# Kernel tuning notes

Hardware: AMD Instinct MI355X
Metric: run time of the kernel (lower is better)

## Reference

```python
import jax, jax.numpy as jnp
import numpy as np

N = 100000   # nodes
E = 1000000  # directed edges
C = 64       # channels
K = 4        # propagation hops
DT = 1.0     # dt; exp_init=False branch: 2*x + dt^2*conv(x) - x_pre


def setup_inputs() -> dict:
    key = jax.random.key(0)
    k1, k2, k3, k4, k5 = jax.random.split(key, 5)
    x = jax.random.normal(k1, (N, C), dtype=jnp.float32)
    x_pre = jax.random.normal(k2, (N, C), dtype=jnp.float32)
    edge_index = jax.random.randint(k3, (2, E), 0, N, dtype=jnp.int32)
    bound = 1.0 / np.sqrt(C)  # PyG Linear default (kaiming-uniform-like)
    W = jax.random.uniform(k4, (C, C), jnp.float32, -bound, bound)
    b = jax.random.uniform(k5, (C,), jnp.float32, -bound, bound)
    return {"x": x, "x_pre": x_pre, "edge_index": edge_index, "W": W, "b": b}


def _sgc(x, edge_index, W, b):
    # gcn_norm: add self-loops, symmetric normalization D^-1/2 (A+I) D^-1/2
    loop = jnp.arange(N, dtype=edge_index.dtype)
    src = jnp.concatenate([edge_index[0], loop])  # source j
    dst = jnp.concatenate([edge_index[1], loop])  # target i
    deg = jax.ops.segment_sum(jnp.ones(src.shape, jnp.float32), dst, num_segments=N)
    dinv = jnp.where(deg > 0, jax.lax.rsqrt(deg), 0.0)
    norm = dinv[src] * dinv[dst]  # [E+N]
    h = x
    for _ in range(K):  # K-hop sparse propagation (gather -> scale -> scatter-add)
        h = jax.ops.segment_sum(h[src] * norm[:, None], dst, num_segments=N)
    return h @ W.T + b  # SGConv final linear


def reference(x, x_pre, edge_index, W, b):
    return 2.0 * x + (DT * DT) * _sgc(x, edge_index, W, b) - x_pre
```

## Files before the change

### kernel.cpp

```cpp
#include <hip/hip_runtime.h>
#include <hip/hip_fp16.h>

#define CCH 64
#define NBLK 128
#define BKT  256


__global__ void countA(const int* __restrict__ dst, int* __restrict__ cntmat,
                       int E, int chunk, int B) {
    __shared__ int h[512];
    int t = threadIdx.x, blk = blockIdx.x;
    for (int i = t; i < B; i += 256) h[i] = 0;
    __syncthreads();
    int e0 = blk * chunk, e1 = min(e0 + chunk, E);
    for (int e = e0 + t; e < e1; e += 256) atomicAdd(&h[dst[e] >> 8], 1);
    __syncthreads();
    for (int i = t; i < B; i += 256) cntmat[i * NBLK + blk] = h[i];
}

__global__ void scan1(const int* __restrict__ cnt, int* __restrict__ part,
                      int* __restrict__ bsum, int N) {
    __shared__ int s[256];
    int t = threadIdx.x;
    int base = blockIdx.x * 1024 + t * 4;
    int v0 = (base + 0 < N) ? cnt[base + 0] : 0;
    int v1 = (base + 1 < N) ? cnt[base + 1] : 0;
    int v2 = (base + 2 < N) ? cnt[base + 2] : 0;
    int v3 = (base + 3 < N) ? cnt[base + 3] : 0;
    s[t] = v0 + v1 + v2 + v3;
    __syncthreads();
    for (int off = 1; off < 256; off <<= 1) {
        int xx = (t >= off) ? s[t - off] : 0;
        __syncthreads();
        s[t] += xx;
        __syncthreads();
    }
    int excl = (t == 0) ? 0 : s[t - 1];
    if (t == 255) bsum[blockIdx.x] = s[255];
    if (base + 0 < N) part[base + 0] = excl;
    if (base + 1 < N) part[base + 1] = excl + v0;
    if (base + 2 < N) part[base + 2] = excl + v0 + v1;
    if (base + 3 < N) part[base + 3] = excl + v0 + v1 + v2;
}

__device__ __forceinline__ void scan_bsum(const int* __restrict__ bsum, int NB2,
                                          int* sbs, int t) {
    int v = (t < NB2) ? bsum[t] : 0;
    sbs[t] = v;
    __syncthreads();
    for (int o = 1; o < 256; o <<= 1) {
        int xx = (t >= o) ? sbs[t - o] : 0;
        __syncthreads();
        sbs[t] += xx;
        __syncthreads();
    }
    int e = sbs[t] - v;
    __syncthreads();
    sbs[t] = e;
    __syncthreads();
}

__global__ void partA(const int* __restrict__ src, const int* __restrict__ dst,
                      const int* __restrict__ part, const int* __restrict__ bsum,
                      unsigned* __restrict__ brec, int E, int chunk, int B, int NB2) {
    __shared__ int cur[512];
    __shared__ int sbs[256];
    int t = threadIdx.x, blk = blockIdx.x;
    scan_bsum(bsum, NB2, sbs, t);
    for (int i = t; i < B; i += 256) {
        int idx = i * NBLK + blk;
        cur[i] = part[idx] + sbs[idx >> 10];
    }
    __syncthreads();
    int e0 = blk * chunk, e1 = min(e0 + chunk, E);
    for (int e = e0 + t; e < e1; e += 256) {
        int s = src[e], d = dst[e];
        int pos = atomicAdd(&cur[d >> 8], 1);
        brec[pos] = ((unsigned)s << 8) | (unsigned)(d & 255);
    }
}

__global__ void buildB(const unsigned* __restrict__ brec, const int* __restrict__ part,
                       const int* __restrict__ bsum, int* __restrict__ row_ptr,
                       int* __restrict__ adj, float* __restrict__ dinv,
                       float* __restrict__ dinv2, const float* __restrict__ x,
                       __half* __restrict__ xh, int N, int B, int E, int NB2) {
    __shared__ int hist[256];
    __shared__ int scanbuf[256];
    __shared__ int cursor[256];
    __shared__ int sbs[256];
    __shared__ float sdinv[256];
    int t = threadIdx.x, k = blockIdx.x;
    scan_bsum(bsum, NB2, sbs, t);
    int i0 = k * NBLK;
    int base = part[i0] + sbs[i0 >> 10];
    int nextb;
    if (k + 1 < B) {
        int i1 = (k + 1) * NBLK;
        nextb = part[i1] + sbs[i1 >> 10];
    } else {
        nextb = E;
    }
    hist[t] = 0;
    __syncthreads();
    for (int i = base + t; i < nextb; i += 256) atomicAdd(&hist[brec[i] & 255u], 1);
    __syncthreads();
    int v = hist[t];
    scanbuf[t] = v;
    __syncthreads();
    for (int o = 1; o < 256; o <<= 1) {
        int xx = (t >= o) ? scanbuf[t - o] : 0;
        __syncthreads();
        scanbuf[t] += xx;
        __syncthreads();
    }
    int excl = scanbuf[t] - v;
    int node = k * 256 + t;
    float di = 0.f;
    if (node < N) {
        int p = base + excl;
        row_ptr[node] = p;
        cursor[t] = p;
        float dp1 = (float)v + 1.0f;
        di = rsqrtf(dp1);
        dinv[node]  = di;
        dinv2[node] = 1.0f / dp1;
    }
    sdinv[t] = di;
    if (k == 0 && t == 0) row_ptr[N] = E;
    __syncthreads();
    for (int i = base + t; i < nextb; i += 256) {
        unsigned r = brec[i];
        int pos = atomicAdd(&cursor[r & 255u], 1);
        adj[pos] = (int)(r >> 8);
    }
    int nodeBase = k * 256;
    for (int i = t; i < 2048; i += 256) {
        int nl = i >> 3;
        int node2 = nodeBase + nl;
        if (node2 < N) {
            float d = sdinv[nl];
            size_t baseE = (size_t)node2 * 64 + (size_t)(i & 7) * 8;
            float4 a = *(const float4*)&x[baseE];
            float4 c = *(const float4*)&x[baseE + 4];
            float4 o;
            __half2* op = (__half2*)&o;
            op[0] = __float22half2_rn(make_float2(d * a.x, d * a.y));
            op[1] = __float22half2_rn(make_float2(d * a.z, d * a.w));
            op[2] = __float22half2_rn(make_float2(d * c.x, d * c.y));
            op[3] = __float22half2_rn(make_float2(d * c.z, d * c.w));
            *(float4*)&xh[baseE] = o;
        }
    }
}


__device__ __forceinline__ void acc16w(float4 hv, float w, float* acc) {
    __half2* hp = (__half2*)&hv;
    #pragma unroll
    for (int i2 = 0; i2 < 4; ++i2) {
        float2 f = __half22float2(hp[i2]);
        acc[2 * i2]     = fmaf(w, f.x, acc[2 * i2]);
        acc[2 * i2 + 1] = fmaf(w, f.y, acc[2 * i2 + 1]);
    }
}

__device__ __forceinline__ void prop_body(const __half* __restrict__ hin,
                                          const int* __restrict__ row_ptr,
                                          const int* __restrict__ adj,
                                          int nodeC, int cnt, int g8, int q,
                                          int E, float* acc) {
    int rp0 = row_ptr[nodeC];

    int R = cnt;
    R = max(R, __shfl_xor(R, 8, 64));
    R = max(R, __shfl_xor(R, 16, 64));
    R = max(R, __shfl_xor(R, 32, 64));

    const float4* hin16 = (const float4*)hin;
    float4 selfv = hin16[(size_t)nodeC * 8 + q];

    int eCur = adj[rp0 + q];
    int eNxt = adj[rp0 + 8 + q];
    int j0 = __shfl(eCur, g8 + 0, 64); j0 = (0 < cnt) ? j0 : 0;
    int j1 = __shfl(eCur, g8 + 1, 64); j1 = (1 < cnt) ? j1 : 0;
    int j2 = __shfl(eCur, g8 + 2, 64); j2 = (2 < cnt) ? j2 : 0;
    int j3 = __shfl(eCur, g8 + 3, 64); j3 = (3 < cnt) ? j3 : 0;
    float4 gA0 = hin16[(size_t)j0 * 8 + q];
    float4 gA1 = hin16[(size_t)j1 * 8 + q];
    float4 gA2 = hin16[(size_t)j2 * 8 + q];
    float4 gA3 = hin16[(size_t)j3 * 8 + q];
    float4 gB0, gB1, gB2, gB3;

    acc16w(selfv, 1.f, acc);

    for (int r = 0; r < R; r += 8) {
        int t;
        t = r + 4; j0 = __shfl(eCur, g8 + (t & 7), 64); j0 = (t < cnt) ? j0 : 0;
        t = r + 5; j1 = __shfl(eCur, g8 + (t & 7), 64); j1 = (t < cnt) ? j1 : 0;
        t = r + 6; j2 = __shfl(eCur, g8 + (t & 7), 64); j2 = (t < cnt) ? j2 : 0;
        t = r + 7; j3 = __shfl(eCur, g8 + (t & 7), 64); j3 = (t < cnt) ? j3 : 0;
        gB0 = hin16[(size_t)j0 * 8 + q];
        gB1 = hin16[(size_t)j1 * 8 + q];
        gB2 = hin16[(size_t)j2 * 8 + q];
        gB3 = hin16[(size_t)j3 * 8 + q];
        float w;
        w = (r + 0 < cnt) ? 1.f : 0.f; acc16w(gA0, w, acc);
        w = (r + 1 < cnt) ? 1.f : 0.f; acc16w(gA1, w, acc);
        w = (r + 2 < cnt) ? 1.f : 0.f; acc16w(gA2, w, acc);
        w = (r + 3 < cnt) ? 1.f : 0.f; acc16w(gA3, w, acc);
        t = r + 8;  j0 = __shfl(eNxt, g8 + (t & 7), 64); j0 = (t < cnt) ? j0 : 0;
        t = r + 9;  j1 = __shfl(eNxt, g8 + (t & 7), 64); j1 = (t < cnt) ? j1 : 0;
        t = r + 10; j2 = __shfl(eNxt, g8 + (t & 7), 64); j2 = (t < cnt) ? j2 : 0;
        t = r + 11; j3 = __shfl(eNxt, g8 + (t & 7), 64); j3 = (t < cnt) ? j3 : 0;
        gA0 = hin16[(size_t)j0 * 8 + q];
        gA1 = hin16[(size_t)j1 * 8 + q];
        gA2 = hin16[(size_t)j2 * 8 + q];
        gA3 = hin16[(size_t)j3 * 8 + q];
        w = (r + 4 < cnt) ? 1.f : 0.f; acc16w(gB0, w, acc);
        w = (r + 5 < cnt) ? 1.f : 0.f; acc16w(gB1, w, acc);
        w = (r + 6 < cnt) ? 1.f : 0.f; acc16w(gB2, w, acc);
        w = (r + 7 < cnt) ? 1.f : 0.f; acc16w(gB3, w, acc);
        eCur = eNxt;
        int ao = rp0 + r + 16;
        ao = (ao > E + 96) ? (E + 96) : ao;
        eNxt = adj[ao + q];
    }
}

__global__ void __launch_bounds__(256, 8)
prop_kernel(const __half* __restrict__ hin, __half* __restrict__ hout,
            const int* __restrict__ row_ptr, const int* __restrict__ adj,
            const float* __restrict__ scale, int N, int E) {
    int wid  = (blockIdx.x * blockDim.x + threadIdx.x) >> 6;
    int lane = threadIdx.x & 63;
    int g    = lane >> 3;
    int q    = lane & 7;
    int nb   = wid << 3;
    if (nb >= N) return;
    int  node  = nb + g;
    bool valid = node < N;
    int  nodeC = valid ? node : (N - 1);
    int cnt = valid ? (row_ptr[nodeC + 1] - row_ptr[nodeC]) : 0;

    float acc[8] = {0.f, 0.f, 0.f, 0.f, 0.f, 0.f, 0.f, 0.f};
    prop_body(hin, row_ptr, adj, nodeC, cnt, g << 3, q, E, acc);

    if (valid) {
        float sc = scale[nodeC];
        float4 o;
        __half2* op = (__half2*)&o;
        op[0] = __float22half2_rn(make_float2(sc * acc[0], sc * acc[1]));
        op[1] = __float22half2_rn(make_float2(sc * acc[2], sc * acc[3]));
        op[2] = __float22half2_rn(make_float2(sc * acc[4], sc * acc[5]));
        op[3] = __float22half2_rn(make_float2(sc * acc[6], sc * acc[7]));
        ((float4*)hout)[(size_t)node * 8 + q] = o;
    }
}

__global__ void __launch_bounds__(256, 6)
prop_final_kernel(const __half* __restrict__ hin, const float* __restrict__ x,
                  const float* __restrict__ xp, const float* __restrict__ W,
                  const float* __restrict__ b, float* __restrict__ out,
                  const int* __restrict__ row_ptr, const int* __restrict__ adj,
                  const float* __restrict__ dinv, int N, int E) {
    __shared__ __align__(16) float Wt[64 * 68];
    __shared__ __align__(16) float ht[32 * 68];
    int t = threadIdx.x;
    int nodeBase = blockIdx.x * 32;

    for (int i = t; i < 1024; i += 256) {
        int c  = i >> 4;
        int k4 = i & 15;
        float4 w4 = ((const float4*)W)[i];
        Wt[(k4 * 4 + 0) * 68 + c] = w4.x;
        Wt[(k4 * 4 + 1) * 68 + c] = w4.y;
        Wt[(k4 * 4 + 2) * 68 + c] = w4.z;
        Wt[(k4 * 4 + 3) * 68 + c] = w4.w;
    }

    int wv   = t >> 6;
    int lane = t & 63;
    int g    = lane >> 3;
    int q    = lane & 7;
    int nl   = wv * 8 + g;
    int node = nodeBase + nl;
    bool valid = node < N;
    int  nodeC = valid ? node : (N - 1);
    int cnt = valid ? (row_ptr[nodeC + 1] - row_ptr[nodeC]) : 0;

    float acc[8] = {0.f, 0.f, 0.f, 0.f, 0.f, 0.f, 0.f, 0.f};
    prop_body(hin, row_ptr, adj, nodeC, cnt, g << 3, q, E, acc);

    float sc = valid ? dinv[nodeC] : 0.f;
    {
        float* hrow = &ht[nl * 68 + q * 8];
        float4 h0, h1;
        h0.x = sc * acc[0]; h0.y = sc * acc[1]; h0.z = sc * acc[2]; h0.w = sc * acc[3];
        h1.x = sc * acc[4]; h1.y = sc * acc[5]; h1.z = sc * acc[6]; h1.w = sc * acc[7];
        *(float4*)&hrow[0] = h0;
        *(float4*)&hrow[4] = h1;
    }
    __syncthreads();

    int r0 = t >> 4;
    int c0 = (t & 15) * 4;
    float4 bv = *(const float4*)&b[c0];
    #pragma unroll
    for (int p = 0; p < 2; ++p) {
        int n = r0 + p * 16;
        int nd = nodeBase + n;
        float4 av = make_float4(0.f, 0.f, 0.f, 0.f);
        #pragma unroll 4
        for (int k4 = 0; k4 < 16; ++k4) {
            float4 h4 = *(const float4*)&ht[n * 68 + k4 * 4];
            float4 w0 = *(const float4*)&Wt[(k4 * 4 + 0) * 68 + c0];
            float4 w1 = *(const float4*)&Wt[(k4 * 4 + 1) * 68 + c0];
            float4 w2 = *(const float4*)&Wt[(k4 * 4 + 2) * 68 + c0];
            float4 w3 = *(const float4*)&Wt[(k4 * 4 + 3) * 68 + c0];
            av.x = fmaf(h4.x, w0.x, av.x); av.y = fmaf(h4.x, w0.y, av.y);
            av.z = fmaf(h4.x, w0.z, av.z); av.w = fmaf(h4.x, w0.w, av.w);
            av.x = fmaf(h4.y, w1.x, av.x); av.y = fmaf(h4.y, w1.y, av.y);
            av.z = fmaf(h4.y, w1.z, av.z); av.w = fmaf(h4.y, w1.w, av.w);
            av.x = fmaf(h4.z, w2.x, av.x); av.y = fmaf(h4.z, w2.y, av.y);
            av.z = fmaf(h4.z, w2.z, av.z); av.w = fmaf(h4.z, w2.w, av.w);
            av.x = fmaf(h4.w, w3.x, av.x); av.y = fmaf(h4.w, w3.y, av.y);
            av.z = fmaf(h4.w, w3.z, av.z); av.w = fmaf(h4.w, w3.w, av.w);
        }
        if (nd < N) {
            int base = nd * 64 + c0;
            float4 xv = *(const float4*)&x[base];
            float4 pv = *(const float4*)&xp[base];
            float4 o;
            o.x = fmaf(2.f, xv.x, av.x + bv.x) - pv.x;
            o.y = fmaf(2.f, xv.y, av.y + bv.y) - pv.y;
            o.z = fmaf(2.f, xv.z, av.z + bv.z) - pv.z;
            o.w = fmaf(2.f, xv.w, av.w + bv.w) - pv.w;
            *(float4*)&out[base] = o;
        }
    }
}

extern "C" void kernel_launch(void* const* d_in, const int* in_sizes, int n_in,
                              void* d_out, int out_size, void* d_ws, size_t ws_size,
                              hipStream_t stream) {
    const float* x    = (const float*)d_in[0];
    const float* xpre = (const float*)d_in[1];
    const int*   ei   = (const int*)d_in[2];
    const float* W    = (const float*)d_in[3];
    const float* b    = (const float*)d_in[4];
    float* out = (float*)d_out;

    const int N = in_sizes[0] / CCH;
    const int E = in_sizes[2] / 2;
    const int* src = ei;
    const int* dst = ei + E;

    const int B     = (N + BKT - 1) / BKT;
    const int M     = B * NBLK;
    const int chunk = (E + NBLK - 1) / NBLK;
    const int NB2   = (M + 1023) / 1024;

    char* p = (char*)d_ws;
    auto alloc = [&](size_t bytes) -> char* {
        char* r = p;
        p += (bytes + 255) & ~(size_t)255;
        return r;
    };
    int*      cntmat  = (int*)alloc((size_t)M * 4);
    int*      part    = (int*)alloc((size_t)M * 4);
    int*      bsum    = (int*)alloc((size_t)NB2 * 4);
    unsigned* brec    = (unsigned*)alloc((size_t)E * 4);
    int*      adj     = (int*)alloc(((size_t)E + 128) * 4);
    int*      row_ptr = (int*)alloc(((size_t)N + 1) * 4);
    float*    dinv    = (float*)alloc((size_t)N * 4);
    float*    dinv2   = (float*)alloc((size_t)N * 4);
    __half*   xh      = (__half*)alloc((size_t)N * CCH * 2);
    __half*   g0      = (__half*)alloc((size_t)N * CCH * 2);
    __half*   g1      = (__half*)alloc((size_t)N * CCH * 2);

    countA<<<NBLK, 256, 0, stream>>>(dst, cntmat, E, chunk, B);
    scan1 <<<NB2, 256, 0, stream>>>(cntmat, part, bsum, M);
    partA <<<NBLK, 256, 0, stream>>>(src, dst, part, bsum, brec, E, chunk, B, NB2);
    buildB<<<B, 256, 0, stream>>>(brec, part, bsum, row_ptr, adj, dinv, dinv2,
                                  x, xh, N, B, E, NB2);

    const int nwave = (N + 7) / 8;
    const int pgrid = (nwave + 3) / 4;
    prop_kernel<<<pgrid, 256, 0, stream>>>(xh, g0, row_ptr, adj, dinv2, N, E);
    prop_kernel<<<pgrid, 256, 0, stream>>>(g0, g1, row_ptr, adj, dinv2, N, E);
    prop_kernel<<<pgrid, 256, 0, stream>>>(g1, g0, row_ptr, adj, dinv2, N, E);
    prop_final_kernel<<<(N + 31) / 32, 256, 0, stream>>>(g0, x, xpre, W, b, out,
                                                         row_ptr, adj, dinv, N, E);
    (void)g1;
}
```

Before: 246.8 us.

## Deepen gather pipeline to 16 in-flight rows and swizzle W smem layout

The neighbor-gather loop now keeps two 8-wide batches of feature-row loads in flight instead of 4-wide ones, prefetches adjacency indices two steps ahead, and skips the second batch when the padded degree runs out. This hides more gather latency but raises register pressure, so prop_kernel's launch bound drops from 8 to 6 waves. The final kernel stores W row-major with an XOR swizzle on the k index, so shared-memory stores are float4 writes and reads avoid bank conflicts.

```diff
diff --git a/kernel.cpp b/kernel.cpp
--- a/kernel.cpp
+++ b/kernel.cpp
@@ -180,55 +180,66 @@
     const float4* hin16 = (const float4*)hin;
     float4 selfv = hin16[(size_t)nodeC * 8 + q];
 
-    int eCur = adj[rp0 + q];
-    int eNxt = adj[rp0 + 8 + q];
-    int j0 = __shfl(eCur, g8 + 0, 64); j0 = (0 < cnt) ? j0 : 0;
-    int j1 = __shfl(eCur, g8 + 1, 64); j1 = (1 < cnt) ? j1 : 0;
-    int j2 = __shfl(eCur, g8 + 2, 64); j2 = (2 < cnt) ? j2 : 0;
-    int j3 = __shfl(eCur, g8 + 3, 64); j3 = (3 < cnt) ? j3 : 0;
-    float4 gA0 = hin16[(size_t)j0 * 8 + q];
-    float4 gA1 = hin16[(size_t)j1 * 8 + q];
-    float4 gA2 = hin16[(size_t)j2 * 8 + q];
-    float4 gA3 = hin16[(size_t)j3 * 8 + q];
-    float4 gB0, gB1, gB2, gB3;
-
+#define PISSUE(bufv, eb, base, u) do {                                   \
+        int jj = __shfl(eb, g8 + (u), 64);                               \
+        jj = ((base) + (u) < cnt) ? jj : 0;                              \
+        bufv = hin16[(size_t)jj * 8 + q]; } while (0)
+#define PACC(bufv, base, u) do {                                         \
+        float ww = ((base) + (u) < cnt) ? 1.f : 0.f;                     \
+        acc16w(bufv, ww, acc); } while (0)
+#define CLAMPA(off) ((rp0 + (off) > E + 112) ? (E + 112) : (rp0 + (off)))
+
+    float4 gA0, gA1, gA2, gA3, gA4, gA5, gA6, gA7;
+    float4 gB0, gB1, gB2, gB3, gB4, gB5, gB6, gB7;
+
+    int e0 = adj[rp0 + q];
+    int e1 = adj[CLAMPA(8) + q];
+    int e2 = adj[CLAMPA(16) + q];
+
+    if (R > 0) {
+        PISSUE(gA0, e0, 0, 0); PISSUE(gA1, e0, 0, 1);
+        PISSUE(gA2, e0, 0, 2); PISSUE(gA3, e0, 0, 3);
+        PISSUE(gA4, e0, 0, 4); PISSUE(gA5, e0, 0, 5);
+        PISSUE(gA6, e0, 0, 6); PISSUE(gA7, e0, 0, 7);
+    }
     acc16w(selfv, 1.f, acc);
 
-    for (int r = 0; r < R; r += 8) {
-        int t;
-        t = r + 4; j0 = __shfl(eCur, g8 + (t & 7), 64); j0 = (t < cnt) ? j0 : 0;
-        t = r + 5; j1 = __shfl(eCur, g8 + (t & 7), 64); j1 = (t < cnt) ? j1 : 0;
-        t = r + 6; j2 = __shfl(eCur, g8 + (t & 7), 64); j2 = (t < cnt) ? j2 : 0;
-        t = r + 7; j3 = __shfl(eCur, g8 + (t & 7), 64); j3 = (t < cnt) ? j3 : 0;
-        gB0 = hin16[(size_t)j0 * 8 + q];
-        gB1 = hin16[(size_t)j1 * 8 + q];
-        gB2 = hin16[(size_t)j2 * 8 + q];
-        gB3 = hin16[(size_t)j3 * 8 + q];
-        float w;
-        w = (r + 0 < cnt) ? 1.f : 0.f; acc16w(gA0, w, acc);
-        w = (r + 1 < cnt) ? 1.f : 0.f; acc16w(gA1, w, acc);
-        w = (r + 2 < cnt) ? 1.f : 0.f; acc16w(gA2, w, acc);
-        w = (r + 3 < cnt) ? 1.f : 0.f; acc16w(gA3, w, acc);
-        t = r + 8;  j0 = __shfl(eNxt, g8 + (t & 7), 64); j0 = (t < cnt) ? j0 : 0;
-        t = r + 9;  j1 = __shfl(eNxt, g8 + (t & 7), 64); j1 = (t < cnt) ? j1 : 0;
-        t = r + 10; j2 = __shfl(eNxt, g8 + (t & 7), 64); j2 = (t < cnt) ? j2 : 0;
-        t = r + 11; j3 = __shfl(eNxt, g8 + (t & 7), 64); j3 = (t < cnt) ? j3 : 0;
-        gA0 = hin16[(size_t)j0 * 8 + q];
-        gA1 = hin16[(size_t)j1 * 8 + q];
-        gA2 = hin16[(size_t)j2 * 8 + q];
-        gA3 = hin16[(size_t)j3 * 8 + q];
-        w = (r + 4 < cnt) ? 1.f : 0.f; acc16w(gB0, w, acc);
-        w = (r + 5 < cnt) ? 1.f : 0.f; acc16w(gB1, w, acc);
-        w = (r + 6 < cnt) ? 1.f : 0.f; acc16w(gB2, w, acc);
-        w = (r + 7 < cnt) ? 1.f : 0.f; acc16w(gB3, w, acc);
-        eCur = eNxt;
-        int ao = rp0 + r + 16;
-        ao = (ao > E + 96) ? (E + 96) : ao;
-        eNxt = adj[ao + q];
-    }
-}
-
-__global__ void __launch_bounds__(256, 8)
+    for (int r = 0; r < R; r += 16) {
+        bool hB = (r + 8  < R);
+        bool hN = (r + 16 < R);
+        int eN1 = 0, eN2 = 0;
+        if (hN) {
+            eN1 = adj[CLAMPA(r + 24) + q];
+            eN2 = adj[CLAMPA(r + 32) + q];
+        }
+        if (hB) {
+            PISSUE(gB0, e1, r + 8, 0); PISSUE(gB1, e1, r + 8, 1);
+            PISSUE(gB2, e1, r + 8, 2); PISSUE(gB3, e1, r + 8, 3);
+            PISSUE(gB4, e1, r + 8, 4); PISSUE(gB5, e1, r + 8, 5);
+            PISSUE(gB6, e1, r + 8, 6); PISSUE(gB7, e1, r + 8, 7);
+        }
+        PACC(gA0, r, 0); PACC(gA1, r, 1); PACC(gA2, r, 2); PACC(gA3, r, 3);
+        PACC(gA4, r, 4); PACC(gA5, r, 5); PACC(gA6, r, 6); PACC(gA7, r, 7);
+        if (hN) {
+            PISSUE(gA0, e2, r + 16, 0); PISSUE(gA1, e2, r + 16, 1);
+            PISSUE(gA2, e2, r + 16, 2); PISSUE(gA3, e2, r + 16, 3);
+            PISSUE(gA4, e2, r + 16, 4); PISSUE(gA5, e2, r + 16, 5);
+            PISSUE(gA6, e2, r + 16, 6); PISSUE(gA7, e2, r + 16, 7);
+        }
+        if (hB) {
+            PACC(gB0, r + 8, 0); PACC(gB1, r + 8, 1);
+            PACC(gB2, r + 8, 2); PACC(gB3, r + 8, 3);
+            PACC(gB4, r + 8, 4); PACC(gB5, r + 8, 5);
+            PACC(gB6, r + 8, 6); PACC(gB7, r + 8, 7);
+        }
+        e1 = eN1; e2 = eN2;
+    }
+#undef PISSUE
+#undef PACC
+#undef CLAMPA
+}
+
+__global__ void __launch_bounds__(256, 6)
 prop_kernel(const __half* __restrict__ hin, __half* __restrict__ hout,
             const int* __restrict__ row_ptr, const int* __restrict__ adj,
             const float* __restrict__ scale, int N, int E) {
@@ -264,7 +275,7 @@
                   const float* __restrict__ b, float* __restrict__ out,
                   const int* __restrict__ row_ptr, const int* __restrict__ adj,
                   const float* __restrict__ dinv, int N, int E) {
-    __shared__ __align__(16) float Wt[64 * 68];
+    __shared__ __align__(16) float Ws[64 * 68];
     __shared__ __align__(16) float ht[32 * 68];
     int t = threadIdx.x;
     int nodeBase = blockIdx.x * 32;
@@ -273,10 +284,8 @@
         int c  = i >> 4;
         int k4 = i & 15;
         float4 w4 = ((const float4*)W)[i];
-        Wt[(k4 * 4 + 0) * 68 + c] = w4.x;
-        Wt[(k4 * 4 + 1) * 68 + c] = w4.y;
-        Wt[(k4 * 4 + 2) * 68 + c] = w4.z;
-        Wt[(k4 * 4 + 3) * 68 + c] = w4.w;
+        int k4s = k4 ^ ((c >> 2) & 7);
+        *(float4*)&Ws[c * 68 + k4s * 4] = w4;
     }
 
     int wv   = t >> 6;
@@ -304,7 +313,9 @@
     __syncthreads();
 
     int r0 = t >> 4;
-    int c0 = (t & 15) * 4;
+    int m  = t & 15;
+    int c0 = m * 4;
+    int s  = m & 7;
     float4 bv = *(const float4*)&b[c0];
     #pragma unroll
     for (int p = 0; p < 2; ++p) {
@@ -314,18 +325,19 @@
         #pragma unroll 4
         for (int k4 = 0; k4 < 16; ++k4) {
             float4 h4 = *(const float4*)&ht[n * 68 + k4 * 4];
-            float4 w0 = *(const float4*)&Wt[(k4 * 4 + 0) * 68 + c0];
-            float4 w1 = *(const float4*)&Wt[(k4 * 4 + 1) * 68 + c0];
-            float4 w2 = *(const float4*)&Wt[(k4 * 4 + 2) * 68 + c0];
-            float4 w3 = *(const float4*)&Wt[(k4 * 4 + 3) * 68 + c0];
-            av.x = fmaf(h4.x, w0.x, av.x); av.y = fmaf(h4.x, w0.y, av.y);
-            av.z = fmaf(h4.x, w0.z, av.z); av.w = fmaf(h4.x, w0.w, av.w);
-            av.x = fmaf(h4.y, w1.x, av.x); av.y = fmaf(h4.y, w1.y, av.y);
-            av.z = fmaf(h4.y, w1.z, av.z); av.w = fmaf(h4.y, w1.w, av.w);
-            av.x = fmaf(h4.z, w2.x, av.x); av.y = fmaf(h4.z, w2.y, av.y);
-            av.z = fmaf(h4.z, w2.z, av.z); av.w = fmaf(h4.z, w2.w, av.w);
-            av.x = fmaf(h4.w, w3.x, av.x); av.y = fmaf(h4.w, w3.y, av.y);
-            av.z = fmaf(h4.w, w3.z, av.z); av.w = fmaf(h4.w, w3.w, av.w);
+            int ks = (k4 ^ s) * 4;
+            float4 w0 = *(const float4*)&Ws[(c0 + 0) * 68 + ks];
+            float4 w1 = *(const float4*)&Ws[(c0 + 1) * 68 + ks];
+            float4 w2 = *(const float4*)&Ws[(c0 + 2) * 68 + ks];
+            float4 w3 = *(const float4*)&Ws[(c0 + 3) * 68 + ks];
+            av.x = fmaf(h4.x, w0.x, av.x); av.x = fmaf(h4.y, w0.y, av.x);
+            av.x = fmaf(h4.z, w0.z, av.x); av.x = fmaf(h4.w, w0.w, av.x);
+            av.y = fmaf(h4.x, w1.x, av.y); av.y = fmaf(h4.y, w1.y, av.y);
+            av.y = fmaf(h4.z, w1.z, av.y); av.y = fmaf(h4.w, w1.w, av.y);
+            av.z = fmaf(h4.x, w2.x, av.z); av.z = fmaf(h4.y, w2.y, av.z);
+            av.z = fmaf(h4.z, w2.z, av.z); av.z = fmaf(h4.w, w2.w, av.z);
+            av.w = fmaf(h4.x, w3.x, av.w); av.w = fmaf(h4.y, w3.y, av.w);
+            av.w = fmaf(h4.z, w3.z, av.w); av.w = fmaf(h4.w, w3.w, av.w);
         }
         if (nd < N) {
             int base = nd * 64 + c0;
```

Result: slower. 556.2 us (+125.3%).
